# Kernel optimization log

Hardware: AMD Instinct MI355X
Metric: run time of the kernel (lower is better)

Reference implementation:

```python
import jax, jax.numpy as jnp
import numpy as np

VOCAB, EDIM, ENC, H, OUT = 50000, 128, 128, 100, 104
B, L, NPT = 128, 64, 64          # batch, statements per seq, nodes per statement tree
N = B * L * NPT                  # 524288 total nodes
MAXD = 6                         # max depth of a 64-node complete binary tree


def setup_inputs() -> dict:
    key = jax.random.key(0)
    ks = jax.random.split(key, 14)
    tokens = jax.random.randint(ks[0], (N,), 0, VOCAB)
    # structured tree topology: each statement tree is a 64-node complete binary tree
    local = np.arange(NPT)
    par_local = np.where(local == 0, 0, (local - 1) // 2)
    depth_local = np.floor(np.log2(local + 1)).astype(np.int32)
    base = np.repeat(np.arange(B * L) * NPT, NPT)
    parent = jnp.asarray(base + np.tile(par_local, B * L), dtype=jnp.int32)
    depth = jnp.asarray(np.tile(depth_local, B * L), dtype=jnp.int32)
    tree_id = jnp.asarray(np.repeat(np.arange(B * L), NPT), dtype=jnp.int32)
    nrm = lambda k, s, sc: jax.random.normal(k, s, jnp.float32) * sc
    return {
        "tokens": tokens, "parent": parent, "depth": depth, "tree_id": tree_id,
        "emb": nrm(ks[1], (VOCAB, EDIM), 0.02),
        "W_lin": nrm(ks[2], (ENC, EDIM), 0.05), "b_lin": nrm(ks[3], (ENC,), 0.05),
        "Wi_f": nrm(ks[4], (3 * H, ENC), 0.05), "Wh_f": nrm(ks[5], (3 * H, H), 0.05),
        "bi_f": nrm(ks[6], (3 * H,), 0.05), "bh_f": nrm(ks[7], (3 * H,), 0.05),
        "Wi_b": nrm(ks[8], (3 * H, ENC), 0.05), "Wh_b": nrm(ks[9], (3 * H, H), 0.05),
        "bi_b": nrm(ks[10], (3 * H,), 0.05), "bh_b": nrm(ks[11], (3 * H,), 0.05),
        "W_fc": nrm(ks[12], (OUT, 2 * H), 0.05), "b_fc": nrm(ks[13], (OUT,), 0.05),
    }


def _gru_scan(x_seq, Wi, Wh, bi, bh):
    # x_seq: [L, B, ENC] -> outputs [L, B, H]. Matches torch.nn.GRU cell math.
    def step(hprev, xt):
        gi = xt @ Wi.T + bi              # [B, 3H]
        gh = hprev @ Wh.T + bh
        ir, iz, inn = jnp.split(gi, 3, axis=-1)
        hr, hz, hn = jnp.split(gh, 3, axis=-1)
        r = jax.nn.sigmoid(ir + hr)
        z = jax.nn.sigmoid(iz + hz)
        n = jnp.tanh(inn + r * hn)
        hnew = (1.0 - z) * n + z * hprev
        return hnew, hnew
    h0 = jnp.zeros((x_seq.shape[1], Wh.shape[1]), x_seq.dtype)
    _, ys = jax.lax.scan(step, h0, x_seq)
    return ys


def reference(tokens, parent, depth, tree_id, emb, W_lin, b_lin,
              Wi_f, Wh_f, bi_f, bh_f, Wi_b, Wh_b, bi_b, bh_b, W_fc, b_fc):
    # per-node value: linear(embedding(token))   [N, ENC]
    h = emb[tokens] @ W_lin.T + b_lin
    # bottom-up subtree sum: h(node) = v(node) + sum(h(children)), batched by depth level
    for d in range(MAXD, 0, -1):
        contrib = jnp.where((depth == d)[:, None], h, 0.0)
        h = h.at[parent].add(contrib)
    # TreeEncoder output: max over all node hidden states of each tree
    encodes = jax.ops.segment_max(h, tree_id, num_segments=B * L)  # [B*L, ENC]
    x = encodes.reshape(B, L, ENC).transpose(1, 0, 2)              # [L, B, ENC]
    yf = _gru_scan(x, Wi_f, Wh_f, bi_f, bh_f)                      # [L, B, H]
    yb = _gru_scan(x[::-1], Wi_b, Wh_b, bi_b, bh_b)[::-1]
    gru_out = jnp.concatenate([yf, yb], axis=-1)                   # [L, B, 2H]
    pooled = gru_out.max(axis=0)                                   # [B, 2H]
    return pooled @ W_fc.T + b_fc                                  # [B, OUT]
```

## Files before the change

kernel.cpp:

```cpp
#include <hip/hip_runtime.h>
#include <hip/hip_bf16.h>

typedef __bf16 bf16_t;
typedef __attribute__((ext_vector_type(8))) __bf16 bf16x8;
typedef __attribute__((ext_vector_type(4))) float f32x4;

#define TREES 8192
#define ENC 128
#define HH 100
#define G3 300
#define GSTRIDE 304
#define BB 128
#define LL 64
#define OUTD 104
#define TPB_TREES 8

__device__ __forceinline__ float sigm(float x) { return 1.0f / (1.0f + __expf(-x)); }
__device__ __forceinline__ float tanh_f(float x) { return 2.0f / (1.0f + __expf(-2.0f * x)) - 1.0f; }

__device__ __forceinline__ int subtree_size(int n) {
  int np1 = n + 1;
  int d = 31 - __clz(np1);
  return ((64 >> d) - 1) + (((np1 & (np1 - 1)) == 0) ? 1 : 0);
}

__global__ __launch_bounds__(256) void k0_prep(const float* __restrict__ W_lin,
                                               const float* __restrict__ Wi_f,
                                               const float* __restrict__ Wi_b,
                                               bf16_t* __restrict__ Wbf,
                                               bf16_t* __restrict__ Wibf) {
  int i = blockIdx.x * 256 + threadIdx.x;
  if (i < 128 * 128) Wbf[i] = (bf16_t)W_lin[i];
  if (i < 608 * 128) {
    int jg = i >> 7, k = i & 127;
    int dir = (jg >= GSTRIDE) ? 1 : 0;
    int j = jg - dir * GSTRIDE;
    float v = 0.0f;
    if (j < G3) v = dir ? Wi_b[j * 128 + k] : Wi_f[j * 128 + k];
    Wibf[i] = (bf16_t)v;
  }
}

__global__ __launch_bounds__(256) void k1_tree(const int* __restrict__ tokens,
                                               const float* __restrict__ emb,
                                               const bf16_t* __restrict__ Wbf,
                                               const float* __restrict__ b_lin,
                                               float* __restrict__ encodes) {
  __shared__ float s[64][132];
  __shared__ float maxbuf[2][128];
  __shared__ float sb[128];
  int tid = threadIdx.x;
  int wave = tid >> 6;
  int lane = tid & 63;
  int ri = lane & 15;
  int kg = lane >> 4;
  int wm = wave >> 1;
  int wn = wave & 1;

  if (tid < 128) sb[tid] = b_lin[tid];

  bf16x8 bfr[4][4];
#pragma unroll
  for (int ks = 0; ks < 4; ++ks)
#pragma unroll
    for (int ni = 0; ni < 4; ++ni)
      bfr[ks][ni] = *(const bf16x8*)(Wbf + (size_t)((wn * 4 + ni) * 16 + ri) * 128 +
                                     ks * 32 + kg * 8);

  float szs[2][4];
#pragma unroll
  for (int mi = 0; mi < 2; ++mi)
#pragma unroll
    for (int rr = 0; rr < 4; ++rr)
      szs[mi][rr] = (float)subtree_size(wm * 32 + mi * 16 + kg * 4 + rr);

  int n = tid >> 2;
  int q = tid & 3;

  for (int t = 0; t < TPB_TREES; ++t) {
    int tree = blockIdx.x * TPB_TREES + t;

    {
      int tok = tokens[tree * 64 + n];
      const float4* src = (const float4*)(emb + (size_t)tok * ENC + q * 32);
#pragma unroll
      for (int i = 0; i < 8; ++i) *(float4*)&s[n][q * 32 + i * 4] = src[i];
    }
    __syncthreads();

    if (tid < 128) s[31][tid] += s[63][tid];
    __syncthreads();
    for (int lev = 4; lev >= 0; --lev) {
      int p0 = (1 << lev) - 1;
      int items = (1 << lev) * 128;
      for (int it = tid; it < items; it += 256) {
        int p = p0 + (it >> 7);
        int c = it & 127;
        s[p][c] += s[2 * p + 1][c] + s[2 * p + 2][c];
      }
      __syncthreads();
    }

    f32x4 acc[2][4];
#pragma unroll
    for (int mi = 0; mi < 2; ++mi)
#pragma unroll
      for (int ni = 0; ni < 4; ++ni) {
        f32x4 z = {0.f, 0.f, 0.f, 0.f};
        acc[mi][ni] = z;
      }
#pragma unroll
    for (int ks = 0; ks < 4; ++ks) {
      int k0 = ks * 32 + kg * 8;
#pragma unroll
      for (int mi = 0; mi < 2; ++mi) {
        float4 a0 = *(const float4*)&s[wm * 32 + mi * 16 + ri][k0];
        float4 a1 = *(const float4*)&s[wm * 32 + mi * 16 + ri][k0 + 4];
        bf16x8 afr;
        afr[0] = (bf16_t)a0.x; afr[1] = (bf16_t)a0.y; afr[2] = (bf16_t)a0.z; afr[3] = (bf16_t)a0.w;
        afr[4] = (bf16_t)a1.x; afr[5] = (bf16_t)a1.y; afr[6] = (bf16_t)a1.z; afr[7] = (bf16_t)a1.w;
#pragma unroll
        for (int ni = 0; ni < 4; ++ni)
          acc[mi][ni] = __builtin_amdgcn_mfma_f32_16x16x32_bf16(afr, bfr[ks][ni], acc[mi][ni], 0, 0, 0);
      }
    }

    float cmax[4];
#pragma unroll
    for (int ni = 0; ni < 4; ++ni) {
      float bl = sb[(wn * 4 + ni) * 16 + ri];
      float m = -1e30f;
#pragma unroll
      for (int mi = 0; mi < 2; ++mi) {
        f32x4 a = acc[mi][ni];
        m = fmaxf(m, fmaxf(fmaxf(a.x + szs[mi][0] * bl, a.y + szs[mi][1] * bl),
                           fmaxf(a.z + szs[mi][2] * bl, a.w + szs[mi][3] * bl)));
      }
      cmax[ni] = m;
    }
#pragma unroll
    for (int off = 16; off < 64; off <<= 1) {
#pragma unroll
      for (int ni = 0; ni < 4; ++ni)
        cmax[ni] = fmaxf(cmax[ni], __shfl_xor(cmax[ni], off));
    }
    if (lane < 16) {
#pragma unroll
      for (int ni = 0; ni < 4; ++ni) maxbuf[wm][(wn * 4 + ni) * 16 + lane] = cmax[ni];
    }
    __syncthreads();
    if (tid < 128) {
      encodes[(size_t)tree * ENC + tid] = fmaxf(maxbuf[0][tid], maxbuf[1][tid]);
    }
    __syncthreads();
  }
}

__global__ __launch_bounds__(256) void k2_gi(const float* __restrict__ encodes,
                                             const bf16_t* __restrict__ Wibf,
                                             const float* __restrict__ bi_f,
                                             const float* __restrict__ bi_b,
                                             float* __restrict__ GI) {
  int tid = threadIdx.x;
  int wave = tid >> 6;
  int lane = tid & 63;
  int ri = lane & 15;
  int kg = lane >> 4;
  int m0 = blockIdx.x * 16;

  f32x4 acc[10];
#pragma unroll
  for (int i = 0; i < 10; ++i) {
    f32x4 z = {0.f, 0.f, 0.f, 0.f};
    acc[i] = z;
  }

  int r = m0 + ri;
  int er = (r & 127) * 64 + (r >> 7);
  const float* arow = encodes + (size_t)er * ENC;
#pragma unroll
  for (int ks = 0; ks < 4; ++ks) {
    int k0 = ks * 32 + kg * 8;
    float4 a0 = *(const float4*)(arow + k0);
    float4 a1 = *(const float4*)(arow + k0 + 4);
    bf16x8 afr;
    afr[0] = (bf16_t)a0.x; afr[1] = (bf16_t)a0.y; afr[2] = (bf16_t)a0.z; afr[3] = (bf16_t)a0.w;
    afr[4] = (bf16_t)a1.x; afr[5] = (bf16_t)a1.y; afr[6] = (bf16_t)a1.z; afr[7] = (bf16_t)a1.w;
#pragma unroll
    for (int i = 0; i < 10; ++i) {
      int nt = wave + i * 4;
      if (nt < 38) {
        bf16x8 bfr = *(const bf16x8*)(Wibf + (nt * 16 + ri) * 128 + k0);
        acc[i] = __builtin_amdgcn_mfma_f32_16x16x32_bf16(afr, bfr, acc[i], 0, 0, 0);
      }
    }
  }
#pragma unroll
  for (int i = 0; i < 10; ++i) {
    int nt = wave + i * 4;
    if (nt >= 38) continue;
    int jg = nt * 16 + ri;
    int dir = (jg >= GSTRIDE) ? 1 : 0;
    int j = jg - dir * GSTRIDE;
    if (j >= G3) continue;
    float bias = dir ? bi_b[j] : bi_f[j];
#pragma unroll
    for (int rr = 0; rr < 4; ++rr) {
      int rowg = m0 + kg * 4 + rr;
      int l = rowg >> 7, b = rowg & 127;
      GI[(((size_t)dir * LL + l) * BB + b) * GSTRIDE + j] = acc[i][rr] + bias;
    }
  }
}

__global__ __launch_bounds__(640) void k3_gru(const float* __restrict__ GI,
                                              const float* __restrict__ Wh_f,
                                              const float* __restrict__ Wh_b,
                                              const float* __restrict__ bh_f,
                                              const float* __restrict__ bh_b,
                                              float* __restrict__ pooled) {
  int blk = blockIdx.x;
  int dir = blk >> 7;
  int b = blk & 127;
  int tid = threadIdx.x;
  __shared__ __align__(16) float h_lds[104];
  __shared__ float gh_lds[304];
  __shared__ float gi_lds[2][304];
  const float* Wh = dir ? Wh_b : Wh_f;
  const float* bh = dir ? bh_b : bh_f;

  int j = tid >> 1;
  int kg = tid & 1;
  int kbase = kg * 52;
  bool isdot = (tid < 600);

  float4 wv[13];
  float bhj = 0.f;
  if (isdot) {
#pragma unroll
    for (int c = 0; c < 13; ++c) {
      int k0 = kbase + c * 4;
      float4 v;
      v.x = (k0 + 0 < HH) ? Wh[j * HH + k0 + 0] : 0.f;
      v.y = (k0 + 1 < HH) ? Wh[j * HH + k0 + 1] : 0.f;
      v.z = (k0 + 2 < HH) ? Wh[j * HH + k0 + 2] : 0.f;
      v.w = (k0 + 3 < HH) ? Wh[j * HH + k0 + 3] : 0.f;
      wv[c] = v;
    }
    if (kg == 0) bhj = bh[j];
  }
  if (tid < 104) h_lds[tid] = 0.f;

  const float* giB = GI + (size_t)dir * LL * BB * GSTRIDE + (size_t)b * GSTRIDE;
  if (tid < G3) {
    int la0 = dir ? 63 : 0;
    gi_lds[0][tid] = giB[(size_t)la0 * BB * GSTRIDE + tid];
  }
  float ymax = -1e30f;
  __syncthreads();

  for (int step = 0; step < 64; ++step) {
    int cur = step & 1;
    int nxt = cur ^ 1;
    float ginext = 0.f;
    if (tid < G3) {
      int ns = (step < 63) ? step + 1 : 63;
      int la = dir ? (63 - ns) : ns;
      ginext = giB[(size_t)la * BB * GSTRIDE + tid];
    }
    if (isdot) {
      float a0 = 0.f, a1 = 0.f, a2 = 0.f, a3 = 0.f;
#pragma unroll
      for (int c = 0; c < 13; ++c) {
        float4 hv = *(const float4*)&h_lds[kbase + c * 4];
        a0 += wv[c].x * hv.x;
        a1 += wv[c].y * hv.y;
        a2 += wv[c].z * hv.z;
        a3 += wv[c].w * hv.w;
      }
      float p = (a0 + a1) + (a2 + a3);
      p += __shfl_xor(p, 1);
      if (kg == 0) gh_lds[j] = p + bhj;
    }
    __syncthreads();
    if (tid < HH) {
      float r = sigm(gi_lds[cur][tid] + gh_lds[tid]);
      float z = sigm(gi_lds[cur][100 + tid] + gh_lds[100 + tid]);
      float n = tanh_f(gi_lds[cur][200 + tid] + r * gh_lds[200 + tid]);
      float hnew = (1.f - z) * n + z * h_lds[tid];
      ymax = fmaxf(ymax, hnew);
      h_lds[tid] = hnew;
    }
    if (tid < G3 && step < 63) gi_lds[nxt][tid] = ginext;
    __syncthreads();
  }
  if (tid < HH) pooled[(size_t)b * 200 + dir * 100 + tid] = ymax;
}

__global__ __launch_bounds__(128) void k4_fc(const float* __restrict__ pooled,
                                             const float* __restrict__ W_fc,
                                             const float* __restrict__ b_fc,
                                             float* __restrict__ out) {
  int b = blockIdx.x;
  int o = threadIdx.x;
  if (o >= OUTD) return;
  const float* p = pooled + (size_t)b * 200;
  const float* w = W_fc + (size_t)o * 200;
  float acc = b_fc[o];
#pragma unroll 8
  for (int j = 0; j < 200; ++j) acc += p[j] * w[j];
  out[(size_t)b * OUTD + o] = acc;
}

extern "C" void kernel_launch(void* const* d_in, const int* in_sizes, int n_in,
                              void* d_out, int out_size, void* d_ws, size_t ws_size,
                              hipStream_t stream) {
  const int* tokens = (const int*)d_in[0];
  const float* emb = (const float*)d_in[4];
  const float* W_lin = (const float*)d_in[5];
  const float* b_lin = (const float*)d_in[6];
  const float* Wi_f = (const float*)d_in[7];
  const float* Wh_f = (const float*)d_in[8];
  const float* bi_f = (const float*)d_in[9];
  const float* bh_f = (const float*)d_in[10];
  const float* Wi_b = (const float*)d_in[11];
  const float* Wh_b = (const float*)d_in[12];
  const float* bi_b = (const float*)d_in[13];
  const float* bh_b = (const float*)d_in[14];
  const float* W_fc = (const float*)d_in[15];
  const float* b_fc = (const float*)d_in[16];

  float* encodes = (float*)d_ws;
  float* GI = encodes + (size_t)TREES * ENC;
  float* pooled = GI + (size_t)2 * LL * BB * GSTRIDE;
  bf16_t* Wbf = (bf16_t*)(pooled + (size_t)BB * 200);
  bf16_t* Wibf = Wbf + 128 * 128;

  k0_prep<<<304, 256, 0, stream>>>(W_lin, Wi_f, Wi_b, Wbf, Wibf);
  k1_tree<<<TREES / TPB_TREES, 256, 0, stream>>>(tokens, emb, Wbf, b_lin, encodes);
  k2_gi<<<512, 256, 0, stream>>>(encodes, Wibf, bi_f, bi_b, GI);
  k3_gru<<<256, 640, 0, stream>>>(GI, Wh_f, Wh_b, bh_f, bh_b, pooled);
  k4_fc<<<BB, 128, 0, stream>>>(pooled, W_fc, b_fc, (float*)d_out);
}
```

Before: 160.7 us.

## Convert embedding table to bf16 and prefetch next tree's gathered rows

Adds a per-call pass in the prep kernel that converts the full embedding table to bf16 into reused workspace. The tree kernel then gathers half-size rows and software-prefetches the next tree's rows into registers while the current tree is reduced. This halves the random-gather bytes and overlaps load latency with compute. In exchange it adds a full-table conversion pass each call and reduces embedding precision before the subtree sums.

```diff
diff --git a/kernel.cpp b/kernel.cpp
--- a/kernel.cpp
+++ b/kernel.cpp
@@ -17,6 +17,8 @@
 
 __device__ __forceinline__ float sigm(float x) { return 1.0f / (1.0f + __expf(-x)); }
 __device__ __forceinline__ float tanh_f(float x) { return 2.0f / (1.0f + __expf(-2.0f * x)) - 1.0f; }
+__device__ __forceinline__ float bflo(unsigned int u) { return __builtin_bit_cast(float, u << 16); }
+__device__ __forceinline__ float bfhi(unsigned int u) { return __builtin_bit_cast(float, u & 0xffff0000u); }
 
 __device__ __forceinline__ int subtree_size(int n) {
   int np1 = n + 1;
@@ -27,9 +29,20 @@
 __global__ __launch_bounds__(256) void k0_prep(const float* __restrict__ W_lin,
                                                const float* __restrict__ Wi_f,
                                                const float* __restrict__ Wi_b,
+                                               const float* __restrict__ emb,
                                                bf16_t* __restrict__ Wbf,
-                                               bf16_t* __restrict__ Wibf) {
+                                               bf16_t* __restrict__ Wibf,
+                                               bf16_t* __restrict__ embbf) {
   int i = blockIdx.x * 256 + threadIdx.x;
+  if (i < 1600000) {
+    float4 v = ((const float4*)emb)[i];
+    ushort4 u;
+    u.x = __builtin_bit_cast(unsigned short, (bf16_t)v.x);
+    u.y = __builtin_bit_cast(unsigned short, (bf16_t)v.y);
+    u.z = __builtin_bit_cast(unsigned short, (bf16_t)v.z);
+    u.w = __builtin_bit_cast(unsigned short, (bf16_t)v.w);
+    ((ushort4*)embbf)[i] = u;
+  }
   if (i < 128 * 128) Wbf[i] = (bf16_t)W_lin[i];
   if (i < 608 * 128) {
     int jg = i >> 7, k = i & 127;
@@ -42,7 +55,7 @@
 }
 
 __global__ __launch_bounds__(256) void k1_tree(const int* __restrict__ tokens,
-                                               const float* __restrict__ emb,
+                                               const bf16_t* __restrict__ embbf,
                                                const bf16_t* __restrict__ Wbf,
                                                const float* __restrict__ b_lin,
                                                float* __restrict__ encodes) {
@@ -76,17 +89,35 @@
 
   int n = tid >> 2;
   int q = tid & 3;
+  int tree0 = blockIdx.x * TPB_TREES;
+
+  uint4 pre[4];
+  {
+    int tok = tokens[tree0 * 64 + n];
+    const uint4* src = (const uint4*)(embbf + (size_t)tok * ENC) + q * 4;
+#pragma unroll
+    for (int i = 0; i < 4; ++i) pre[i] = src[i];
+  }
 
   for (int t = 0; t < TPB_TREES; ++t) {
-    int tree = blockIdx.x * TPB_TREES + t;
-
-    {
-      int tok = tokens[tree * 64 + n];
-      const float4* src = (const float4*)(emb + (size_t)tok * ENC + q * 32);
-#pragma unroll
-      for (int i = 0; i < 8; ++i) *(float4*)&s[n][q * 32 + i * 4] = src[i];
-    }
-    __syncthreads();
+    int tree = tree0 + t;
+
+#pragma unroll
+    for (int i = 0; i < 4; ++i) {
+      uint4 p = pre[i];
+      float4 f0 = {bflo(p.x), bfhi(p.x), bflo(p.y), bfhi(p.y)};
+      float4 f1 = {bflo(p.z), bfhi(p.z), bflo(p.w), bfhi(p.w)};
+      *(float4*)&s[n][q * 32 + i * 8] = f0;
+      *(float4*)&s[n][q * 32 + i * 8 + 4] = f1;
+    }
+    __syncthreads();
+
+    if (t + 1 < TPB_TREES) {
+      int tok = tokens[(tree + 1) * 64 + n];
+      const uint4* src = (const uint4*)(embbf + (size_t)tok * ENC) + q * 4;
+#pragma unroll
+      for (int i = 0; i < 4; ++i) pre[i] = src[i];
+    }
 
     if (tid < 128) s[31][tid] += s[63][tid];
     __syncthreads();
@@ -335,9 +366,10 @@
   float* pooled = GI + (size_t)2 * LL * BB * GSTRIDE;
   bf16_t* Wbf = (bf16_t*)(pooled + (size_t)BB * 200);
   bf16_t* Wibf = Wbf + 128 * 128;
-
-  k0_prep<<<304, 256, 0, stream>>>(W_lin, Wi_f, Wi_b, Wbf, Wibf);
-  k1_tree<<<TREES / TPB_TREES, 256, 0, stream>>>(tokens, emb, Wbf, b_lin, encodes);
+  bf16_t* embbf = (bf16_t*)GI;
+
+  k0_prep<<<6250, 256, 0, stream>>>(W_lin, Wi_f, Wi_b, emb, Wbf, Wibf, embbf);
+  k1_tree<<<TREES / TPB_TREES, 256, 0, stream>>>(tokens, embbf, Wbf, b_lin, encodes);
   k2_gi<<<512, 256, 0, stream>>>(encodes, Wibf, bi_f, bi_b, GI);
   k3_gru<<<256, 640, 0, stream>>>(GI, Wh_f, Wh_b, bh_f, bh_b, pooled);
   k4_fc<<<BB, 128, 0, stream>>>(pooled, W_fc, b_fc, (float*)d_out);
```

Measured after the change: 160.1 us. No clear change (-0.4%).
